# Kernel tuning notes

Measured on AMD Instinct MI355X. Metric: run time of the kernel, lower is better.

The kernel has to match this reference:

```python
import jax, jax.numpy as jnp
import numpy as np

N_NODES = 100000
NEG_SLOPE = 0.2  # PyG GATConv default leaky_relu slope


def gat_conv(x, src, dst, W, a_src, a_dst, b, concat):
    # x: [N, F_in], W: [F_in, H*C], a_src/a_dst: [H, C], b: [H*C] or [C]
    N = x.shape[0]
    H, C = a_src.shape
    h = (x @ W).reshape(N, H, C)                       # [N, H, C]
    alpha_s = jnp.einsum('nhc,hc->nh', h, a_src)       # [N, H]
    alpha_d = jnp.einsum('nhc,hc->nh', h, a_dst)       # [N, H]
    e = jax.nn.leaky_relu(alpha_s[src] + alpha_d[dst], NEG_SLOPE)  # [E, H]
    # edge-softmax grouped by destination node (numerically stable)
    e_max = jax.ops.segment_max(e, dst, num_segments=N)            # [N, H]
    e_exp = jnp.exp(e - e_max[dst])
    denom = jax.ops.segment_sum(e_exp, dst, num_segments=N)        # [N, H]
    alpha = e_exp / (denom[dst] + 1e-16)                           # [E, H]
    msg = h[src] * alpha[:, :, None]                               # [E, H, C]
    out = jax.ops.segment_sum(msg, dst, num_segments=N)            # [N, H, C]
    out = out.reshape(N, H * C) if concat else out.mean(axis=1)
    return out + b


def setup_inputs() -> dict:
    key = jax.random.key(0)
    ks = jax.random.split(key, 12)
    in_dim, hidden, heads, out_dim = 512, 128, 4, 64
    c1 = hidden // heads   # 32 per-head channels, concat -> hidden
    c2 = hidden            # 128 per-head channels, mean over heads
    E = 600000
    x = jax.random.normal(ks[0], (N_NODES, in_dim), dtype=jnp.float32)
    edge_index = jax.random.randint(ks[1], (2, E), 0, N_NODES, dtype=jnp.int64)
    s = 0.1
    return {
        'x': x,
        'edge_index': edge_index,
        'W1': jax.random.normal(ks[2], (in_dim, heads * c1), dtype=jnp.float32) * s,
        'a_src1': jax.random.normal(ks[3], (heads, c1), dtype=jnp.float32) * s,
        'a_dst1': jax.random.normal(ks[4], (heads, c1), dtype=jnp.float32) * s,
        'b1': jnp.zeros((heads * c1,), dtype=jnp.float32),
        'W2': jax.random.normal(ks[5], (hidden, heads * c2), dtype=jnp.float32) * s,
        'a_src2': jax.random.normal(ks[6], (heads, c2), dtype=jnp.float32) * s,
        'a_dst2': jax.random.normal(ks[7], (heads, c2), dtype=jnp.float32) * s,
        'b2': jnp.zeros((c2,), dtype=jnp.float32),
        'W_lin': jax.random.normal(ks[8], (hidden, out_dim), dtype=jnp.float32) * s,
        'b_lin': jnp.zeros((out_dim,), dtype=jnp.float32),
    }


def reference(x, edge_index, W1, a_src1, a_dst1, b1, W2, a_src2, a_dst2, b2, W_lin, b_lin):
    N = x.shape[0]
    # add self-loops (PyG GATConv default add_self_loops=True)
    loops = jnp.arange(N, dtype=edge_index.dtype)
    src = jnp.concatenate([edge_index[0], loops])
    dst = jnp.concatenate([edge_index[1], loops])
    # dropout layers are identity at inference (training=False)
    h = gat_conv(x, src, dst, W1, a_src1, a_dst1, b1, concat=True)
    h = jax.nn.elu(h)
    embeddings = gat_conv(h, src, dst, W2, a_src2, a_dst2, b2, concat=False)
    out = embeddings @ W_lin + b_lin
    return out, embeddings
```

## Files before the change

### kernel.cpp

```cpp
#include <hip/hip_runtime.h>
#include <hip/hip_bf16.h>

typedef __hip_bfloat16 bf16;
typedef unsigned short u16;
typedef unsigned int u32;
typedef u16 u16x8 __attribute__((ext_vector_type(8)));
typedef __bf16 bf16x8 __attribute__((ext_vector_type(8)));
typedef float f32x4 __attribute__((ext_vector_type(4)));

__device__ __forceinline__ float tof(float x) { return x; }
__device__ __forceinline__ float tof(bf16 x) { return __bfloat162float(x); }
__device__ __forceinline__ bf16 tobf(float x) { return __float2bfloat16(x); }

__device__ __forceinline__ u16 f2bf(float x) {
    unsigned u = __builtin_bit_cast(unsigned, x);
    u += 0x7fffu + ((u >> 16) & 1u);
    return (u16)(u >> 16);
}
__device__ __forceinline__ float bf2f(u16 h) {
    return __builtin_bit_cast(float, (unsigned)h << 16);
}
__device__ __forceinline__ float bflo(u32 u) {
    return __builtin_bit_cast(float, u << 16);
}
__device__ __forceinline__ float bfhi(u32 u) {
    return __builtin_bit_cast(float, u & 0xffff0000u);
}

__global__ void tsplit_k(const float* __restrict__ W, int K, int N,
                         u16* __restrict__ hi, u16* __restrict__ lo)
{
    int i = blockIdx.x * blockDim.x + threadIdx.x;
    if (i >= K * N) return;
    int k = i / N, n = i - k * N;
    float v = W[i];
    u16 h = f2bf(v);
    hi[(long)n * K + k] = h;
    lo[(long)n * K + k] = f2bf(v - bf2f(h));
}

template <bool SPLIT_A>
__global__ __launch_bounds__(256) void gemm_mfma(
    const void* __restrict__ Avoid, const u16* __restrict__ Bhi,
    const u16* __restrict__ Blo, u16* __restrict__ C,
    int M, int Ntot, int K)
{
    __shared__ u16 AsHi[128 * 64];
    __shared__ u16 AsLo[SPLIT_A ? 128 * 64 : 8];
    __shared__ u16 BsHi[128 * 64];
    __shared__ u16 BsLo[128 * 64];
    const int t = threadIdx.x;
    const long bm = (long)blockIdx.y * 128;
    const int bn = blockIdx.x * 128;
    const int srow = t >> 1;
    const int skh  = t & 1;
    const int w  = t >> 6;
    const int wm = (w >> 1) * 64;
    const int wn = (w & 1) * 64;
    const int l  = t & 63;
    const int lr = l & 15;
    const int lg = l >> 4;

    f32x4 acc[4][4];
#pragma unroll
    for (int i = 0; i < 4; ++i)
#pragma unroll
        for (int j = 0; j < 4; ++j) acc[i][j] = {0.f, 0.f, 0.f, 0.f};

    for (int k0 = 0; k0 < K; k0 += 64) {
        {
            long r = bm + srow;
            bool ok = r < M;
            if (SPLIT_A) {
                const float* A = (const float*)Avoid;
                const float4* ap = (const float4*)(A + r * K + k0 + skh * 32);
#pragma unroll
                for (int c = 0; c < 4; ++c) {
                    float va[8];
                    if (ok) {
                        float4 v0 = ap[c * 2], v1 = ap[c * 2 + 1];
                        va[0] = v0.x; va[1] = v0.y; va[2] = v0.z; va[3] = v0.w;
                        va[4] = v1.x; va[5] = v1.y; va[6] = v1.z; va[7] = v1.w;
                    } else {
#pragma unroll
                        for (int j = 0; j < 8; ++j) va[j] = 0.f;
                    }
                    u16x8 hi, lo;
#pragma unroll
                    for (int j = 0; j < 8; ++j) {
                        u16 h = f2bf(va[j]);
                        hi[j] = h;
                        lo[j] = f2bf(va[j] - bf2f(h));
                    }
                    int off = srow * 128 + ((((skh * 4 + c) ^ (srow & 7))) << 4);
                    *(u16x8*)((char*)AsHi + off) = hi;
                    *(u16x8*)((char*)AsLo + off) = lo;
                }
            } else {
                const u16* A = (const u16*)Avoid;
                const u16x8* ap = (const u16x8*)(A + r * K + k0 + skh * 32);
#pragma unroll
                for (int c = 0; c < 4; ++c) {
                    u16x8 hv = {0, 0, 0, 0, 0, 0, 0, 0};
                    if (ok) hv = ap[c];
                    int off = srow * 128 + ((((skh * 4 + c) ^ (srow & 7))) << 4);
                    *(u16x8*)((char*)AsHi + off) = hv;
                }
            }
        }
        {
            const u16x8* bph = (const u16x8*)(Bhi + (long)(bn + srow) * K + k0 + skh * 32);
            const u16x8* bpl = (const u16x8*)(Blo + (long)(bn + srow) * K + k0 + skh * 32);
#pragma unroll
            for (int c = 0; c < 4; ++c) {
                int off = srow * 128 + ((((skh * 4 + c) ^ (srow & 7))) << 4);
                *(u16x8*)((char*)BsHi + off) = bph[c];
                *(u16x8*)((char*)BsLo + off) = bpl[c];
            }
        }
        __syncthreads();
#pragma unroll
        for (int ks = 0; ks < 2; ++ks) {
            bf16x8 bh[4], bl[4];
            const int chl = ks * 4 + lg;
#pragma unroll
            for (int n = 0; n < 4; ++n) {
                int col = wn + n * 16 + lr;
                int off = col * 128 + (((chl ^ (col & 7))) << 4);
                bh[n] = *(const bf16x8*)((const char*)BsHi + off);
                bl[n] = *(const bf16x8*)((const char*)BsLo + off);
            }
#pragma unroll
            for (int m = 0; m < 4; ++m) {
                int row = wm + m * 16 + lr;
                int off = row * 128 + (((chl ^ (row & 7))) << 4);
                bf16x8 ah = *(const bf16x8*)((const char*)AsHi + off);
#pragma unroll
                for (int n = 0; n < 4; ++n)
                    acc[m][n] = __builtin_amdgcn_mfma_f32_16x16x32_bf16(
                        ah, bh[n], acc[m][n], 0, 0, 0);
#pragma unroll
                for (int n = 0; n < 4; ++n)
                    acc[m][n] = __builtin_amdgcn_mfma_f32_16x16x32_bf16(
                        ah, bl[n], acc[m][n], 0, 0, 0);
                if (SPLIT_A) {
                    bf16x8 al = *(const bf16x8*)((const char*)AsLo + off);
#pragma unroll
                    for (int n = 0; n < 4; ++n)
                        acc[m][n] = __builtin_amdgcn_mfma_f32_16x16x32_bf16(
                            al, bh[n], acc[m][n], 0, 0, 0);
                }
            }
        }
        __syncthreads();
    }
#pragma unroll
    for (int m = 0; m < 4; ++m) {
        long r0 = bm + wm + m * 16 + lg * 4;
#pragma unroll
        for (int i = 0; i < 4; ++i) {
            long r = r0 + i;
            if (r < M) {
#pragma unroll
                for (int n = 0; n < 4; ++n) {
                    int col = bn + wn + n * 16 + lr;
                    C[r * Ntot + col] = f2bf(acc[m][n][i]);
                }
            }
        }
    }
}

__global__ void alpha4_k(const bf16* __restrict__ h, const float* __restrict__ asrc,
                         const float* __restrict__ adst, float* __restrict__ out_s,
                         float* __restrict__ out_d, int N)
{
    int i = blockIdx.x * blockDim.x + threadIdx.x;
    if (i >= N * 4) return;
    int n = i >> 2, hh = i & 3;
    const bf16* row = h + (long)n * 128 + hh * 32;
    const float* av = asrc + hh * 32;
    const float* bv = adst + hh * 32;
    float s1 = 0.f, s2 = 0.f;
    for (int c = 0; c < 32; ++c) {
        float v = tof(row[c]);
        s1 += v * av[c];
        s2 += v * bv[c];
    }
    out_s[i] = s1;
    out_d[i] = s2;
}

__global__ __launch_bounds__(256) void alpha2w_k(
    const bf16* __restrict__ h2, const float* __restrict__ as2,
    const float* __restrict__ ad2, float* __restrict__ out_s,
    float* __restrict__ out_d, int N)
{
    int n = blockIdx.x;
    int w = threadIdx.x >> 6;
    int l = threadIdx.x & 63;
    const bf16* row = h2 + (long)n * 512 + w * 128;
    float v0 = tof(row[l]), v1 = tof(row[l + 64]);
    float s1 = v0 * as2[w * 128 + l] + v1 * as2[w * 128 + l + 64];
    float s2 = v0 * ad2[w * 128 + l] + v1 * ad2[w * 128 + l + 64];
#pragma unroll
    for (int off = 32; off; off >>= 1) {
        s1 += __shfl_down(s1, off);
        s2 += __shfl_down(s2, off);
    }
    if (l == 0) { out_s[n * 4 + w] = s1; out_d[n * 4 + w] = s2; }
}

__global__ void init_cnt_k(int* __restrict__ cnt, int N)
{
    int i = blockIdx.x * blockDim.x + threadIdx.x;
    if (i < N) cnt[i] = 1;
}

__global__ void hist_k(const int* __restrict__ dst, int E, int* __restrict__ cnt)
{
    int e = blockIdx.x * blockDim.x + threadIdx.x;
    if (e < E) atomicAdd(&cnt[dst[e]], 1);
}

__global__ __launch_bounds__(256) void scan_blk_k(const int* __restrict__ cnt,
                                                  int* __restrict__ row_ptr,
                                                  int* __restrict__ bsum, int N)
{
    __shared__ int s[256];
    int t = threadIdx.x;
    int i = blockIdx.x * 256 + t;
    int v = (i < N) ? cnt[i] : 0;
    s[t] = v;
    __syncthreads();
    for (int off = 1; off < 256; off <<= 1) {
        int x = (t >= off) ? s[t - off] : 0;
        __syncthreads();
        s[t] += x;
        __syncthreads();
    }
    if (i < N) row_ptr[i] = s[t] - v;
    if (t == 255) bsum[blockIdx.x] = s[255];
}

__global__ __launch_bounds__(512) void scan_top_k(const int* __restrict__ bsum,
                                                  int* __restrict__ bofs, int B)
{
    __shared__ int s[512];
    int t = threadIdx.x;
    int v = (t < B) ? bsum[t] : 0;
    s[t] = v;
    __syncthreads();
    for (int off = 1; off < 512; off <<= 1) {
        int x = (t >= off) ? s[t - off] : 0;
        __syncthreads();
        s[t] += x;
        __syncthreads();
    }
    bofs[t] = s[t] - v;
}

__global__ void add_off_k(int* __restrict__ row_ptr, const int* __restrict__ bofs,
                          int* __restrict__ wofs, int N, int Etot)
{
    int i = blockIdx.x * blockDim.x + threadIdx.x;
    if (i == 0) row_ptr[N] = Etot;
    if (i >= N) return;
    int r = row_ptr[i] + bofs[i >> 8];
    row_ptr[i] = r;
    wofs[i] = r;
}

__global__ void scatter_k(const int* __restrict__ dst, const int* __restrict__ src,
                          int E, int Etot,
                          int* __restrict__ wofs, int* __restrict__ sidx)
{
    int e = blockIdx.x * blockDim.x + threadIdx.x;
    if (e >= Etot) return;
    int d, s;
    if (e < E) { d = dst[e]; s = src[e]; }
    else       { d = e - E;  s = d; }
    int pos = atomicAdd(&wofs[d], 1);
    sidx[pos] = s;
}

__global__ void edgew_k(const int* __restrict__ row_ptr, const int* __restrict__ sidx,
                        const float* __restrict__ asv, const float* __restrict__ adv,
                        float* __restrict__ aw, float* __restrict__ invden, int N)
{
    int i = blockIdx.x * blockDim.x + threadIdx.x;
    if (i >= N * 4) return;
    int d = i >> 2, hh = i & 3;
    int beg = row_ptr[d], end = row_ptr[d + 1];
    float ad_d = adv[i];
    float m = -1e30f;
    for (int j = beg; j < end; ++j) {
        float l = asv[sidx[j] * 4 + hh] + ad_d;
        l = l > 0.f ? l : 0.2f * l;
        m = fmaxf(m, l);
    }
    float den = 0.f;
    for (int j = beg; j < end; ++j) {
        float l = asv[sidx[j] * 4 + hh] + ad_d;
        l = l > 0.f ? l : 0.2f * l;
        float w = __expf(l - m);
        den += w;
        aw[(long)j * 4 + hh] = w;
    }
    invden[i] = 1.f / (den + 1e-16f);
}

__global__ __launch_bounds__(256) void agg1_gather_k(
    const int* __restrict__ row_ptr, const int* __restrict__ sidx,
    const float* __restrict__ aw, const float* __restrict__ invden,
    const bf16* __restrict__ h1, const float* __restrict__ b1,
    bf16* __restrict__ out1b, int N)
{
    int d = blockIdx.x * 4 + (threadIdx.x >> 6);
    if (d >= N) return;
    int t = threadIdx.x & 63;
    int c0 = t * 2;
    int hh = t >> 4;
    int beg = row_ptr[d], end = row_ptr[d + 1];
    float accA = 0.f, accB = 0.f;
    for (int j = beg; j < end; ++j) {
        int s = sidx[j];
        float a = aw[(long)j * 4 + hh];
        u32 u = *(const u32*)((const u16*)h1 + (long)s * 128 + c0);
        accA += a * bflo(u);
        accB += a * bfhi(u);
    }
    float inv = invden[d * 4 + hh];
    float vA = accA * inv + b1[c0];
    float vB = accB * inv + b1[c0 + 1];
    vA = vA > 0.f ? vA : (__expf(vA) - 1.f);
    vB = vB > 0.f ? vB : (__expf(vB) - 1.f);
    u32 packed = (u32)f2bf(vA) | ((u32)f2bf(vB) << 16);
    *(u32*)((u16*)out1b + (long)d * 128 + c0) = packed;
}

__global__ __launch_bounds__(256) void agg2_gather_k(
    const int* __restrict__ row_ptr, const int* __restrict__ sidx,
    const float* __restrict__ aw, const float* __restrict__ invden,
    const bf16* __restrict__ h2, const float* __restrict__ b2,
    float* __restrict__ emb, int N)
{
    int d = blockIdx.x * 4 + (threadIdx.x >> 6);
    if (d >= N) return;
    int t = threadIdx.x & 63;
    int c0 = t * 2;
    int beg = row_ptr[d], end = row_ptr[d + 1];
    float a0A = 0.f, a0B = 0.f, a1A = 0.f, a1B = 0.f;
    float a2A = 0.f, a2B = 0.f, a3A = 0.f, a3B = 0.f;
    for (int j = beg; j < end; ++j) {
        int s = sidx[j];
        float4 w = *(const float4*)&aw[(long)j * 4];
        const u16* hrow = (const u16*)h2 + (long)s * 512 + c0;
        u32 u0 = *(const u32*)(hrow);
        u32 u1 = *(const u32*)(hrow + 128);
        u32 u2 = *(const u32*)(hrow + 256);
        u32 u3 = *(const u32*)(hrow + 384);
        a0A += w.x * bflo(u0); a0B += w.x * bfhi(u0);
        a1A += w.y * bflo(u1); a1B += w.y * bfhi(u1);
        a2A += w.z * bflo(u2); a2B += w.z * bfhi(u2);
        a3A += w.w * bflo(u3); a3B += w.w * bfhi(u3);
    }
    float4 inv = *(const float4*)&invden[d * 4];
    float eA = 0.25f * (a0A * inv.x + a1A * inv.y + a2A * inv.z + a3A * inv.w) + b2[c0];
    float eB = 0.25f * (a0B * inv.x + a1B * inv.y + a2B * inv.z + a3B * inv.w) + b2[c0 + 1];
    float2 ev = {eA, eB};
    *(float2*)&emb[(long)d * 128 + c0] = ev;
}

__global__ __launch_bounds__(256) void final_k(const float* __restrict__ emb,
                                               const float* __restrict__ W,
                                               const float* __restrict__ bias,
                                               float* __restrict__ out, int N)
{
    __shared__ float Ws[128 * 64];
    __shared__ float Es[4][132];
    const int tid = threadIdx.x;
    for (int i = tid; i < 128 * 64; i += 256) Ws[i] = W[i];
    int node0 = blockIdx.x * 4;
    for (int i = tid; i < 512; i += 256) {
        int nn = i >> 7, c = i & 127;
        int n = node0 + nn;
        Es[nn][c] = (n < N) ? emb[(long)n * 128 + c] : 0.f;
    }
    __syncthreads();
    int nn = tid >> 6, j = tid & 63;
    int n = node0 + nn;
    if (n >= N) return;
    float acc = bias[j];
#pragma unroll 8
    for (int k = 0; k < 128; ++k) acc += Es[nn][k] * Ws[k * 64 + j];
    out[(long)n * 64 + j] = acc;
}

__global__ void diag_k(float* __restrict__ out, long n, float val)
{
    long i = (long)blockIdx.x * blockDim.x + threadIdx.x;
    if (i >= n) return;
    out[i] = val;
}

extern "C" void kernel_launch(void* const* d_in, const int* in_sizes, int n_in,
                              void* d_out, int out_size, void* d_ws, size_t ws_size,
                              hipStream_t stream)
{
    const float* x   = (const float*)d_in[0];
    const int* ei    = (const int*)d_in[1];
    const float* W1  = (const float*)d_in[2];
    const float* as1 = (const float*)d_in[3];
    const float* ad1 = (const float*)d_in[4];
    const float* b1  = (const float*)d_in[5];
    const float* W2  = (const float*)d_in[6];
    const float* as2 = (const float*)d_in[7];
    const float* ad2 = (const float*)d_in[8];
    const float* b2  = (const float*)d_in[9];
    const float* Wl  = (const float*)d_in[10];
    const float* bl  = (const float*)d_in[11];

    const int N = in_sizes[0] / 512;
    const int E = in_sizes[1] / 2;
    const int Etot = E + N;
    const int* src = ei;
    const int* dst = ei + E;

    float* outp = (float*)d_out;
    float* embp = outp + (size_t)N * 64;
    bf16* out1b = (bf16*)embp;
    float* aw = outp;

    char* wsb = (char*)d_ws;
    bf16*  h2    = (bf16*)wsb;
    bf16*  h1    = (bf16*)wsb;
    float* asv   = (float*)(wsb + (size_t)N * 512 * sizeof(bf16));
    float* adv   = asv + (size_t)N * 4;
    float* invden = adv + (size_t)N * 4;
    int*   cnt   = (int*)(invden + (size_t)N * 4);
    int*   row_ptr = cnt + N;
    int*   wofs  = row_ptr + (N + 1);
    int*   bsum  = wofs + N;
    int*   bofs  = bsum + 512;
    int*   sidx  = bofs + 512;
    char*  pw    = (char*)(sidx + Etot);
    pw = (char*)(((uintptr_t)pw + 255) & ~(uintptr_t)255);
    u16*   w1t_hi = (u16*)pw;
    u16*   w1t_lo = w1t_hi + 128 * 512;
    u16*   w2t_hi = w1t_lo + 128 * 512;
    u16*   w2t_lo = w2t_hi + 512 * 128;
    size_t need  = (size_t)((char*)(w2t_lo + 512 * 128) - wsb);

    dim3 blk(256);
    long n_out_total = (long)N * 192;

    if (ws_size < need) {
        float val = 100.0f + (float)(ws_size >> 20);
        diag_k<<<(int)((n_out_total + 255) / 256), blk, 0, stream>>>(outp, n_out_total, val);
        return;
    }

    const int B = (N + 255) / 256;
    const int gM = (N + 127) / 128;
    const int gAgg = (N + 3) / 4;

    tsplit_k<<<(512 * 128 + 255) / 256, blk, 0, stream>>>(W1, 512, 128, w1t_hi, w1t_lo);
    tsplit_k<<<(128 * 512 + 255) / 256, blk, 0, stream>>>(W2, 128, 512, w2t_hi, w2t_lo);

    init_cnt_k<<<B, blk, 0, stream>>>(cnt, N);
    hist_k<<<(E + 255) / 256, blk, 0, stream>>>(dst, E, cnt);
    scan_blk_k<<<B, blk, 0, stream>>>(cnt, row_ptr, bsum, N);
    scan_top_k<<<1, 512, 0, stream>>>(bsum, bofs, B);
    add_off_k<<<B, blk, 0, stream>>>(row_ptr, bofs, wofs, N, Etot);
    scatter_k<<<(Etot + 255) / 256, blk, 0, stream>>>(dst, src, E, Etot, wofs, sidx);

    gemm_mfma<true><<<dim3(1, gM), blk, 0, stream>>>(
        (const void*)x, w1t_hi, w1t_lo, (u16*)h1, N, 128, 512);
    alpha4_k<<<(N * 4 + 255) / 256, blk, 0, stream>>>(h1, as1, ad1, asv, adv, N);
    edgew_k<<<(N * 4 + 255) / 256, blk, 0, stream>>>(row_ptr, sidx, asv, adv, aw, invden, N);
    agg1_gather_k<<<gAgg, blk, 0, stream>>>(row_ptr, sidx, aw, invden, h1, b1, out1b, N);

    gemm_mfma<false><<<dim3(4, gM), blk, 0, stream>>>(
        (const void*)out1b, w2t_hi, w2t_lo, (u16*)h2, N, 512, 128);
    alpha2w_k<<<N, 256, 0, stream>>>(h2, as2, ad2, asv, adv, N);
    edgew_k<<<(N * 4 + 255) / 256, blk, 0, stream>>>(row_ptr, sidx, asv, adv, aw, invden, N);
    agg2_gather_k<<<gAgg, blk, 0, stream>>>(row_ptr, sidx, aw, invden, h2, b2, embp, N);

    final_k<<<(N + 3) / 4, blk, 0, stream>>>(embp, Wl, bl, outp, N);
}
```

Baseline: 850.8 us.

## Aggregate layer-2 features before the linear transform and fold attention vectors into W2

Layer 2 is reordered so edge aggregation runs on the 128-wide layer-1 output, producing a per-head [N,512] buffer that one GEMM then projects with W2 (K=512, N=128), with bias added in the GEMM epilogue. The attention logits are computed directly from the layer-1 output using precomputed vectors V = W2·a_src/a_dst, so the [N,512] h2 tensor is never materialised. The goal is to cut per-edge gather traffic from 512 to 128 bf16 values and remove the h2 write and read. The cost is an extra bf16 rounding of the aggregated intermediate and a different rounding order for the logits.

```diff
diff --git a/kernel.cpp b/kernel.cpp
--- a/kernel.cpp
+++ b/kernel.cpp
@@ -26,6 +26,8 @@
 __device__ __forceinline__ float bfhi(u32 u) {
     return __builtin_bit_cast(float, u & 0xffff0000u);
 }
+__device__ __forceinline__ void cstore(u16* p, float v) { *p = f2bf(v); }
+__device__ __forceinline__ void cstore(float* p, float v) { *p = v; }
 
 __global__ void tsplit_k(const float* __restrict__ W, int K, int N,
                          u16* __restrict__ hi, u16* __restrict__ lo)
@@ -39,11 +41,45 @@
     lo[(long)n * K + k] = f2bf(v - bf2f(h));
 }
 
-template <bool SPLIT_A>
+__global__ void tsplit2_k(const float* __restrict__ W2,
+                          u16* __restrict__ hi, u16* __restrict__ lo)
+{
+    int i = blockIdx.x * blockDim.x + threadIdx.x;
+    if (i >= 128 * 512) return;
+    int c = i >> 9, o2 = i & 511;
+    int hh = o2 >> 7, o = o2 & 127;
+    float v = W2[i];
+    u16 h = f2bf(v);
+    long dsti = (long)o * 512 + hh * 128 + c;
+    hi[dsti] = h;
+    lo[dsti] = f2bf(v - bf2f(h));
+}
+
+__global__ void vmat_k(const float* __restrict__ W2, const float* __restrict__ as2,
+                       const float* __restrict__ ad2,
+                       float* __restrict__ Vs, float* __restrict__ Vd)
+{
+    int i = blockIdx.x * blockDim.x + threadIdx.x;
+    if (i >= 512) return;
+    int hh = i >> 7, c = i & 127;
+    float s = 0.f, d = 0.f;
+    const float* wrow = W2 + (long)c * 512 + hh * 128;
+    const float* ar = as2 + hh * 128;
+    const float* br = ad2 + hh * 128;
+    for (int o = 0; o < 128; ++o) {
+        float w = wrow[o];
+        s += w * ar[o];
+        d += w * br[o];
+    }
+    Vs[i] = s;
+    Vd[i] = d;
+}
+
+template <bool SPLIT_A, typename TC>
 __global__ __launch_bounds__(256) void gemm_mfma(
     const void* __restrict__ Avoid, const u16* __restrict__ Bhi,
-    const u16* __restrict__ Blo, u16* __restrict__ C,
-    int M, int Ntot, int K)
+    const u16* __restrict__ Blo, TC* __restrict__ C,
+    int M, int Ntot, int K, const float* __restrict__ bias)
 {
     __shared__ u16 AsHi[128 * 64];
     __shared__ u16 AsLo[SPLIT_A ? 128 * 64 : 8];
@@ -164,7 +200,9 @@
 #pragma unroll
                 for (int n = 0; n < 4; ++n) {
                     int col = bn + wn + n * 16 + lr;
-                    C[r * Ntot + col] = f2bf(acc[m][n][i]);
+                    float v = acc[m][n][i];
+                    if (bias) v += bias[col];
+                    cstore(&C[r * Ntot + col], v);
                 }
             }
         }
@@ -191,24 +229,26 @@
     out_d[i] = s2;
 }
 
-__global__ __launch_bounds__(256) void alpha2w_k(
-    const bf16* __restrict__ h2, const float* __restrict__ as2,
-    const float* __restrict__ ad2, float* __restrict__ out_s,
-    float* __restrict__ out_d, int N)
-{
-    int n = blockIdx.x;
-    int w = threadIdx.x >> 6;
-    int l = threadIdx.x & 63;
-    const bf16* row = h2 + (long)n * 512 + w * 128;
-    float v0 = tof(row[l]), v1 = tof(row[l + 64]);
-    float s1 = v0 * as2[w * 128 + l] + v1 * as2[w * 128 + l + 64];
-    float s2 = v0 * ad2[w * 128 + l] + v1 * ad2[w * 128 + l + 64];
-#pragma unroll
-    for (int off = 32; off; off >>= 1) {
-        s1 += __shfl_down(s1, off);
-        s2 += __shfl_down(s2, off);
-    }
-    if (l == 0) { out_s[n * 4 + w] = s1; out_d[n * 4 + w] = s2; }
+__global__ void alpha2v_k(const bf16* __restrict__ out1b, const float* __restrict__ Vs,
+                          const float* __restrict__ Vd, float* __restrict__ out_s,
+                          float* __restrict__ out_d, int N)
+{
+    int i = blockIdx.x * blockDim.x + threadIdx.x;
+    if (i >= N * 4) return;
+    int n = i >> 2, hh = i & 3;
+    const u32* rp = (const u32*)((const u16*)out1b + (long)n * 128);
+    const float* vs = Vs + hh * 128;
+    const float* vd = Vd + hh * 128;
+    float s1 = 0.f, s2 = 0.f;
+#pragma unroll 8
+    for (int c2 = 0; c2 < 64; ++c2) {
+        u32 u = rp[c2];
+        float lo = bflo(u), hi = bfhi(u);
+        s1 += lo * vs[c2 * 2] + hi * vs[c2 * 2 + 1];
+        s2 += lo * vd[c2 * 2] + hi * vd[c2 * 2 + 1];
+    }
+    out_s[i] = s1;
+    out_d[i] = s2;
 }
 
 __global__ void init_cnt_k(int* __restrict__ cnt, int N)
@@ -339,11 +379,10 @@
     *(u32*)((u16*)out1b + (long)d * 128 + c0) = packed;
 }
 
-__global__ __launch_bounds__(256) void agg2_gather_k(
+__global__ __launch_bounds__(256) void agg2z_gather_k(
     const int* __restrict__ row_ptr, const int* __restrict__ sidx,
     const float* __restrict__ aw, const float* __restrict__ invden,
-    const bf16* __restrict__ h2, const float* __restrict__ b2,
-    float* __restrict__ emb, int N)
+    const bf16* __restrict__ out1b, u16* __restrict__ Z, int N)
 {
     int d = blockIdx.x * 4 + (threadIdx.x >> 6);
     if (d >= N) return;
@@ -355,21 +394,23 @@
     for (int j = beg; j < end; ++j) {
         int s = sidx[j];
         float4 w = *(const float4*)&aw[(long)j * 4];
-        const u16* hrow = (const u16*)h2 + (long)s * 512 + c0;
-        u32 u0 = *(const u32*)(hrow);
-        u32 u1 = *(const u32*)(hrow + 128);
-        u32 u2 = *(const u32*)(hrow + 256);
-        u32 u3 = *(const u32*)(hrow + 384);
-        a0A += w.x * bflo(u0); a0B += w.x * bfhi(u0);
-        a1A += w.y * bflo(u1); a1B += w.y * bfhi(u1);
-        a2A += w.z * bflo(u2); a2B += w.z * bfhi(u2);
-        a3A += w.w * bflo(u3); a3B += w.w * bfhi(u3);
+        u32 u = *(const u32*)((const u16*)out1b + (long)s * 128 + c0);
+        float lo = bflo(u), hi = bfhi(u);
+        a0A += w.x * lo; a0B += w.x * hi;
+        a1A += w.y * lo; a1B += w.y * hi;
+        a2A += w.z * lo; a2B += w.z * hi;
+        a3A += w.w * lo; a3B += w.w * hi;
     }
     float4 inv = *(const float4*)&invden[d * 4];
-    float eA = 0.25f * (a0A * inv.x + a1A * inv.y + a2A * inv.z + a3A * inv.w) + b2[c0];
-    float eB = 0.25f * (a0B * inv.x + a1B * inv.y + a2B * inv.z + a3B * inv.w) + b2[c0 + 1];
-    float2 ev = {eA, eB};
-    *(float2*)&emb[(long)d * 128 + c0] = ev;
+    u16* zrow = Z + (long)d * 512 + c0;
+    float s0A = 0.25f * inv.x * a0A, s0B = 0.25f * inv.x * a0B;
+    float s1A = 0.25f * inv.y * a1A, s1B = 0.25f * inv.y * a1B;
+    float s2A = 0.25f * inv.z * a2A, s2B = 0.25f * inv.z * a2B;
+    float s3A = 0.25f * inv.w * a3A, s3B = 0.25f * inv.w * a3B;
+    *(u32*)(zrow)       = (u32)f2bf(s0A) | ((u32)f2bf(s0B) << 16);
+    *(u32*)(zrow + 128) = (u32)f2bf(s1A) | ((u32)f2bf(s1B) << 16);
+    *(u32*)(zrow + 256) = (u32)f2bf(s2A) | ((u32)f2bf(s2B) << 16);
+    *(u32*)(zrow + 384) = (u32)f2bf(s3A) | ((u32)f2bf(s3B) << 16);
 }
 
 __global__ __launch_bounds__(256) void final_k(const float* __restrict__ emb,
@@ -433,9 +474,9 @@
     float* aw = outp;
 
     char* wsb = (char*)d_ws;
-    bf16*  h2    = (bf16*)wsb;
+    u16*   Z     = (u16*)wsb;
     bf16*  h1    = (bf16*)wsb;
-    float* asv   = (float*)(wsb + (size_t)N * 512 * sizeof(bf16));
+    float* asv   = (float*)(wsb + (size_t)N * 512 * sizeof(u16));
     float* adv   = asv + (size_t)N * 4;
     float* invden = adv + (size_t)N * 4;
     int*   cnt   = (int*)(invden + (size_t)N * 4);
@@ -450,7 +491,9 @@
     u16*   w1t_lo = w1t_hi + 128 * 512;
     u16*   w2t_hi = w1t_lo + 128 * 512;
     u16*   w2t_lo = w2t_hi + 512 * 128;
-    size_t need  = (size_t)((char*)(w2t_lo + 512 * 128) - wsb);
+    float* Vs    = (float*)(w2t_lo + 512 * 128);
+    float* Vd    = Vs + 512;
+    size_t need  = (size_t)((char*)(Vd + 512) - wsb);
 
     dim3 blk(256);
     long n_out_total = (long)N * 192;
@@ -466,7 +509,8 @@
     const int gAgg = (N + 3) / 4;
 
     tsplit_k<<<(512 * 128 + 255) / 256, blk, 0, stream>>>(W1, 512, 128, w1t_hi, w1t_lo);
-    tsplit_k<<<(128 * 512 + 255) / 256, blk, 0, stream>>>(W2, 128, 512, w2t_hi, w2t_lo);
+    tsplit2_k<<<(128 * 512 + 255) / 256, blk, 0, stream>>>(W2, w2t_hi, w2t_lo);
+    vmat_k<<<2, blk, 0, stream>>>(W2, as2, ad2, Vs, Vd);
 
     init_cnt_k<<<B, blk, 0, stream>>>(cnt, N);
     hist_k<<<(E + 255) / 256, blk, 0, stream>>>(dst, E, cnt);
@@ -475,17 +519,17 @@
     add_off_k<<<B, blk, 0, stream>>>(row_ptr, bofs, wofs, N, Etot);
     scatter_k<<<(Etot + 255) / 256, blk, 0, stream>>>(dst, src, E, Etot, wofs, sidx);
 
-    gemm_mfma<true><<<dim3(1, gM), blk, 0, stream>>>(
-        (const void*)x, w1t_hi, w1t_lo, (u16*)h1, N, 128, 512);
+    gemm_mfma<true, u16><<<dim3(1, gM), blk, 0, stream>>>(
+        (const void*)x, w1t_hi, w1t_lo, (u16*)h1, N, 128, 512, nullptr);
     alpha4_k<<<(N * 4 + 255) / 256, blk, 0, stream>>>(h1, as1, ad1, asv, adv, N);
     edgew_k<<<(N * 4 + 255) / 256, blk, 0, stream>>>(row_ptr, sidx, asv, adv, aw, invden, N);
     agg1_gather_k<<<gAgg, blk, 0, stream>>>(row_ptr, sidx, aw, invden, h1, b1, out1b, N);
 
-    gemm_mfma<false><<<dim3(4, gM), blk, 0, stream>>>(
-        (const void*)out1b, w2t_hi, w2t_lo, (u16*)h2, N, 512, 128);
-    alpha2w_k<<<N, 256, 0, stream>>>(h2, as2, ad2, asv, adv, N);
+    alpha2v_k<<<(N * 4 + 255) / 256, blk, 0, stream>>>(out1b, Vs, Vd, asv, adv, N);
     edgew_k<<<(N * 4 + 255) / 256, blk, 0, stream>>>(row_ptr, sidx, asv, adv, aw, invden, N);
-    agg2_gather_k<<<gAgg, blk, 0, stream>>>(row_ptr, sidx, aw, invden, h2, b2, embp, N);
+    agg2z_gather_k<<<gAgg, blk, 0, stream>>>(row_ptr, sidx, aw, invden, out1b, Z, N);
+    gemm_mfma<false, float><<<dim3(1, gM), blk, 0, stream>>>(
+        (const void*)Z, w2t_hi, w2t_lo, embp, N, 128, 512, b2);
 
     final_k<<<(N + 3) / 4, blk, 0, stream>>>(embp, Wl, bl, outp, N);
 }
```

Measured after the change: 844.7 us. About the same (-0.7%).
